# Optimization experiments

Measured on AMD Instinct MI355X. Metric: run time of the kernel, lower is better.

## Reference

```python
import jax, jax.numpy as jnp
import numpy as np

B, T, D, V, E = 128, 256, 1024, 32000, 300


def setup_inputs() -> dict:
    key = jax.random.key(0)
    ks = jax.random.split(key, 9)
    s = lambda d: 1.0 / np.sqrt(d)
    return {
        "input_to_decoder": jax.random.randint(ks[0], (B, 1), 0, V),
        "encoder_output": jax.random.normal(ks[1], (B, T, D), jnp.float32) * s(D),
        "state_h": jax.random.normal(ks[2], (B, D), jnp.float32) * s(D),
        "state_c": jax.random.normal(ks[3], (B, D), jnp.float32) * s(D),
        "emb_table": jax.random.normal(ks[4], (V, E), jnp.float32) * 0.02,
        "W_lstm": jax.random.normal(ks[5], (D + E, 4 * D), jnp.float32) * s(D + E),
        "U_lstm": jax.random.normal(ks[6], (D, 4 * D), jnp.float32) * s(D),
        "b_lstm": jnp.zeros((4 * D,), jnp.float32),
        "W_dense": jax.random.normal(ks[7], (D, V), jnp.float32) * s(D),
        "b_dense": jnp.zeros((V,), jnp.float32),
    }


def reference(input_to_decoder, encoder_output, state_h, state_c,
              emb_table, W_lstm, U_lstm, b_lstm, W_dense, b_dense):
    # embedding lookup + squeeze(axis=1): [B,1] -> [B,E]
    emb = emb_table[input_to_decoder[:, 0]]
    # Bahdanau-style dot scores: [B,T]
    scores = jnp.einsum("btd,bd->bt", encoder_output, state_h)
    # NOTE: faithful to source - context uses RAW (pre-softmax) scores
    context = jnp.einsum("btd,bt->bd", encoder_output, scores)  # [B,D]
    attention_weights = jax.nn.softmax(scores, axis=1)[..., None]  # [B,T,1]
    # concat context + embedding, single LSTM cell step (Keras gate order i,f,g,o)
    x = jnp.concatenate([context, emb], axis=1)  # [B,D+E]
    z = x @ W_lstm + state_h @ U_lstm + b_lstm  # [B,4D]
    zi, zf, zg, zo = jnp.split(z, 4, axis=1)
    c_new = jax.nn.sigmoid(zf) * state_c + jax.nn.sigmoid(zi) * jnp.tanh(zg)
    h_new = jax.nn.sigmoid(zo) * jnp.tanh(c_new)
    logits = h_new @ W_dense + b_dense  # [B,V]
    return logits, h_new, c_new, attention_weights, context
```

## Files before the change

### kernel.cpp

```cpp
#include <hip/hip_runtime.h>
#include <hip/hip_bf16.h>
#include <cmath>


#define Bc 128
#define Tc 256
#define Dc 1024
#define Vc 32000
#define Ec 300
#define KREAL 2348
#define KXP 2816
#define KSPLIT 4
#define N4 4096

typedef __attribute__((ext_vector_type(8))) short bf16x8;
typedef __attribute__((ext_vector_type(4))) float f32x4;

static __device__ __forceinline__ short f2bf(float x) {
    __hip_bfloat16 b = __float2bfloat16(x);
    return *reinterpret_cast<short*>(&b);
}
static __device__ __forceinline__ unsigned pack2(float a, float b) {
    return (unsigned)(unsigned short)f2bf(a) | ((unsigned)(unsigned short)f2bf(b) << 16);
}

__global__ void k_att1(const float* __restrict__ enc, const float* __restrict__ h,
                       float* __restrict__ scores_g, float* __restrict__ ctx_part) {
    const int tc = blockIdx.x;
    const int b  = blockIdx.y;
    const int tid = threadIdx.x;
    const int wave = tid >> 6, lane = tid & 63;
    __shared__ float s_acc[4][1024];

    const float4* h4 = (const float4*)(h + ((size_t)b << 10));
    float4 hv0 = h4[lane], hv1 = h4[lane + 64], hv2 = h4[lane + 128], hv3 = h4[lane + 192];

    float4 a0 = {0,0,0,0}, a1 = {0,0,0,0}, a2 = {0,0,0,0}, a3 = {0,0,0,0};
    const int t0 = (tc << 6) + (wave << 4);
    const float4* e4 = (const float4*)(enc + ((size_t)(b * Tc + t0) << 10));

    #pragma unroll 2
    for (int i = 0; i < 16; ++i) {
        float4 e0 = e4[lane], e1 = e4[lane + 64], e2 = e4[lane + 128], e3 = e4[lane + 192];
        e4 += 256;
        float d = e0.x*hv0.x + e0.y*hv0.y + e0.z*hv0.z + e0.w*hv0.w
                + e1.x*hv1.x + e1.y*hv1.y + e1.z*hv1.z + e1.w*hv1.w
                + e2.x*hv2.x + e2.y*hv2.y + e2.z*hv2.z + e2.w*hv2.w
                + e3.x*hv3.x + e3.y*hv3.y + e3.z*hv3.z + e3.w*hv3.w;
        #pragma unroll
        for (int off = 32; off; off >>= 1) d += __shfl_xor(d, off, 64);
        if (lane == 0) scores_g[(b << 8) + t0 + i] = d;
        a0.x += d*e0.x; a0.y += d*e0.y; a0.z += d*e0.z; a0.w += d*e0.w;
        a1.x += d*e1.x; a1.y += d*e1.y; a1.z += d*e1.z; a1.w += d*e1.w;
        a2.x += d*e2.x; a2.y += d*e2.y; a2.z += d*e2.z; a2.w += d*e2.w;
        a3.x += d*e3.x; a3.y += d*e3.y; a3.z += d*e3.z; a3.w += d*e3.w;
    }

    *(float4*)&s_acc[wave][lane << 2]         = a0;
    *(float4*)&s_acc[wave][256 + (lane << 2)] = a1;
    *(float4*)&s_acc[wave][512 + (lane << 2)] = a2;
    *(float4*)&s_acc[wave][768 + (lane << 2)] = a3;
    __syncthreads();
    float4 r0 = *(const float4*)&s_acc[0][tid << 2];
    float4 r1 = *(const float4*)&s_acc[1][tid << 2];
    float4 r2 = *(const float4*)&s_acc[2][tid << 2];
    float4 r3 = *(const float4*)&s_acc[3][tid << 2];
    float4 r;
    r.x = r0.x + r1.x + r2.x + r3.x;
    r.y = r0.y + r1.y + r2.y + r3.y;
    r.z = r0.z + r1.z + r2.z + r3.z;
    r.w = r0.w + r1.w + r2.w + r3.w;
    *(float4*)(ctx_part + (((size_t)(tc << 7) + b) << 10) + (tid << 2)) = r;
}

__global__ void k_att2(const float* __restrict__ ctx_part, const float* __restrict__ scores_g,
                       const int* __restrict__ idx, const float* __restrict__ emb_table,
                       const float* __restrict__ h,
                       float* __restrict__ ctx_out, float* __restrict__ attn_out,
                       unsigned short* __restrict__ x_bf) {
    const int b = blockIdx.x;
    const int tid = threadIdx.x;
    __shared__ float red[256];

    float4 cv = {0.f, 0.f, 0.f, 0.f};
    #pragma unroll
    for (int tc = 0; tc < 4; ++tc) {
        float4 s = *(const float4*)(ctx_part + (((size_t)(tc << 7) + b) << 10) + (tid << 2));
        cv.x += s.x; cv.y += s.y; cv.z += s.z; cv.w += s.w;
    }
    *(float4*)(ctx_out + ((size_t)b << 10) + (tid << 2)) = cv;

    unsigned short* xb = x_bf + (size_t)b * KXP;
    uint2 p0; p0.x = pack2(cv.x, cv.y); p0.y = pack2(cv.z, cv.w);
    *(uint2*)&xb[tid << 2] = p0;

    int row = idx[b];
    for (int i = tid; i < Ec; i += 256)
        xb[Dc + i] = (unsigned short)f2bf(emb_table[(size_t)row * Ec + i]);

    float4 hv = *(const float4*)(h + ((size_t)b << 10) + (tid << 2));
    uint2 p1; p1.x = pack2(hv.x, hv.y); p1.y = pack2(hv.z, hv.w);
    *(uint2*)&xb[(Dc + Ec) + (tid << 2)] = p1;

    for (int i = tid; i < KXP - KREAL; i += 256) xb[KREAL + i] = 0;

    float v = scores_g[(b << 8) + tid];
    red[tid] = v;
    __syncthreads();
    for (int s = 128; s; s >>= 1) { if (tid < s) red[tid] = fmaxf(red[tid], red[tid + s]); __syncthreads(); }
    float m = red[0];
    __syncthreads();
    float e = __expf(v - m);
    red[tid] = e;
    __syncthreads();
    for (int s = 128; s; s >>= 1) { if (tid < s) red[tid] += red[tid + s]; __syncthreads(); }
    attn_out[(b << 8) + tid] = e / red[0];
}

__global__ __launch_bounds__(512) void k_zgemm_mfma(
        const unsigned short* __restrict__ xbf, const float* __restrict__ Wl,
        const float* __restrict__ Ul, float* __restrict__ z_part) {
    __shared__ __align__(16) short blds[2 * 8 * 64 * 8];
    const int tid  = threadIdx.x;
    const int wid  = tid >> 6;
    const int lane = tid & 63;
    const int g    = lane >> 4;
    const int r    = lane & 15;
    const int n0   = blockIdx.x << 6;
    const int ksp  = blockIdx.y;

    const int pr = tid >> 4;
    const int c  = tid & 15;
    const int kk = (pr << 1) & 31;
    const int gg = kk >> 3, jj = kk & 7;
    const int ks0 = pr >> 4;

    f32x4 acc[4] = {};
    const unsigned short* xrow = xbf + (size_t)((wid << 4) + r) * KXP;

    float4 wra[2], wrb[2];
    bf16x8 areg[2][2];

    auto loadWU = [&](int gk) -> float4 {
        if (gk < 1324) return *(const float4*)(Wl + (size_t)gk * N4 + n0 + (c << 2));
        if (gk < KREAL) return *(const float4*)(Ul + (size_t)(gk - 1324) * N4 + n0 + (c << 2));
        return float4{0.f, 0.f, 0.f, 0.f};
    };

    {
        const int kt = (ksp * 11) << 6;
        wra[0] = loadWU(kt + (pr << 1));
        wrb[0] = loadWU(kt + (pr << 1) + 1);
        areg[0][0] = *(const bf16x8*)&xrow[kt + (g << 3)];
        areg[0][1] = *(const bf16x8*)&xrow[kt + 32 + (g << 3)];
    }

    #pragma unroll
    for (int t = 0; t < 11; ++t) {
        const int cur = t & 1;
        const int coff = cur << 12;
        {
            const float av[4] = {wra[cur].x, wra[cur].y, wra[cur].z, wra[cur].w};
            const float bv[4] = {wrb[cur].x, wrb[cur].y, wrb[cur].z, wrb[cur].w};
            #pragma unroll
            for (int i = 0; i < 4; ++i) {
                int n = (c << 2) + i;
                int nt = n >> 4;
                int inner = (gg << 4) | (n & 15);
                int Xs = ((((ks0 << 2) + nt) << 6) | inner) ^ nt;
                *(unsigned*)&blds[coff + (Xs << 3) + jj] = pack2(av[i], bv[i]);
            }
        }
        if (t < 10) {
            const int kt = ((ksp * 11) + t + 1) << 6;
            wra[cur ^ 1] = loadWU(kt + (pr << 1));
            wrb[cur ^ 1] = loadWU(kt + (pr << 1) + 1);
            areg[cur ^ 1][0] = *(const bf16x8*)&xrow[kt + (g << 3)];
            areg[cur ^ 1][1] = *(const bf16x8*)&xrow[kt + 32 + (g << 3)];
        }
        __syncthreads();
        #pragma unroll
        for (int ks = 0; ks < 2; ++ks) {
            #pragma unroll
            for (int nt = 0; nt < 4; ++nt) {
                int Xs = ((((ks << 2) + nt) << 6) | lane) ^ nt;
                bf16x8 bfr = *(const bf16x8*)&blds[coff + (Xs << 3)];
                acc[nt] = __builtin_amdgcn_mfma_f32_16x16x32_bf16(areg[cur][ks], bfr, acc[nt], 0, 0, 0);
            }
        }
        __syncthreads();
    }

    float* zp = z_part + ((size_t)ksp << 19);
    #pragma unroll
    for (int nt = 0; nt < 4; ++nt) {
        int col = n0 + (nt << 4) + r;
        #pragma unroll
        for (int j = 0; j < 4; ++j) {
            int rowm = (wid << 4) + (g << 2) + j;
            zp[((size_t)rowm << 12) + col] = acc[nt][j];
        }
    }
}

__global__ void k_gates(const float* __restrict__ z_part, const float* __restrict__ b_lstm,
                        const float* __restrict__ c_in, float* __restrict__ h_new,
                        float* __restrict__ c_new, unsigned short* __restrict__ h_bf) {
    int i = blockIdx.x * 256 + threadIdx.x;
    int b = i >> 8, d4 = (i & 255) << 2;
    size_t base = ((size_t)b << 12) + d4;
    float4 zi = *(const float4*)(b_lstm + d4);
    float4 zf = *(const float4*)(b_lstm + d4 + 1024);
    float4 zg = *(const float4*)(b_lstm + d4 + 2048);
    float4 zo = *(const float4*)(b_lstm + d4 + 3072);
    #pragma unroll
    for (int ks = 0; ks < KSPLIT; ++ks) {
        const float* zp = z_part + ((size_t)ks << 19);
        float4 t;
        t = *(const float4*)(zp + base);        zi.x += t.x; zi.y += t.y; zi.z += t.z; zi.w += t.w;
        t = *(const float4*)(zp + base + 1024); zf.x += t.x; zf.y += t.y; zf.z += t.z; zf.w += t.w;
        t = *(const float4*)(zp + base + 2048); zg.x += t.x; zg.y += t.y; zg.z += t.z; zg.w += t.w;
        t = *(const float4*)(zp + base + 3072); zo.x += t.x; zo.y += t.y; zo.z += t.z; zo.w += t.w;
    }
    float4 cin = *(const float4*)(c_in + ((size_t)b << 10) + d4);
    float4 cn, hn;
    {
        float si = 1.f/(1.f+__expf(-zi.x)), sf = 1.f/(1.f+__expf(-zf.x)), so = 1.f/(1.f+__expf(-zo.x));
        cn.x = sf*cin.x + si*tanhf(zg.x); hn.x = so*tanhf(cn.x);
        si = 1.f/(1.f+__expf(-zi.y)); sf = 1.f/(1.f+__expf(-zf.y)); so = 1.f/(1.f+__expf(-zo.y));
        cn.y = sf*cin.y + si*tanhf(zg.y); hn.y = so*tanhf(cn.y);
        si = 1.f/(1.f+__expf(-zi.z)); sf = 1.f/(1.f+__expf(-zf.z)); so = 1.f/(1.f+__expf(-zo.z));
        cn.z = sf*cin.z + si*tanhf(zg.z); hn.z = so*tanhf(cn.z);
        si = 1.f/(1.f+__expf(-zi.w)); sf = 1.f/(1.f+__expf(-zf.w)); so = 1.f/(1.f+__expf(-zo.w));
        cn.w = sf*cin.w + si*tanhf(zg.w); hn.w = so*tanhf(cn.w);
    }
    *(float4*)(c_new + ((size_t)b << 10) + d4) = cn;
    *(float4*)(h_new + ((size_t)b << 10) + d4) = hn;
    uint2 hp; hp.x = pack2(hn.x, hn.y); hp.y = pack2(hn.z, hn.w);
    *(uint2*)&h_bf[((size_t)b << 10) + d4] = hp;
}

__global__ __launch_bounds__(512, 4) void k_logits_mfma(
        const unsigned short* __restrict__ hbf, const float* __restrict__ Wd,
        const float* __restrict__ bd, float* __restrict__ out) {
    __shared__ __align__(16) short blds[2 * 16 * 64 * 8];
    const int tid  = threadIdx.x;
    const int wid  = tid >> 6;
    const int lane = tid & 63;
    const int g    = lane >> 4;
    const int r    = lane & 15;
    const int n0   = blockIdx.x << 6;

    const int pr = tid >> 4;
    const int c  = tid & 15;
    const int kk = (pr << 1) & 31;
    const int gg = kk >> 3, jj = kk & 7;
    const int ksA = pr >> 4;
    const int ksB = ksA + 2;

    f32x4 acc[4] = {};
    const unsigned short* hrow = hbf + ((size_t)((wid << 4) + r) << 10);
    const float* wbase = Wd + (size_t)(pr << 1) * Vc + n0 + (c << 2);

    float4 wra[2], wrb[2], wrc[2], wrd[2];
    bf16x8 areg[2][4];

    {
        wra[0] = *(const float4*)(wbase);
        wrb[0] = *(const float4*)(wbase + Vc);
        wrc[0] = *(const float4*)(wbase + (size_t)64 * Vc);
        wrd[0] = *(const float4*)(wbase + (size_t)65 * Vc);
        #pragma unroll
        for (int ks = 0; ks < 4; ++ks)
            areg[0][ks] = *(const bf16x8*)&hrow[(ks << 5) + (g << 3)];
    }

    #pragma unroll
    for (int t = 0; t < 8; ++t) {
        const int cur = t & 1;
        const int coff = cur << 13;
        {
            const float a0[4] = {wra[cur].x, wra[cur].y, wra[cur].z, wra[cur].w};
            const float b0[4] = {wrb[cur].x, wrb[cur].y, wrb[cur].z, wrb[cur].w};
            const float c0[4] = {wrc[cur].x, wrc[cur].y, wrc[cur].z, wrc[cur].w};
            const float d0[4] = {wrd[cur].x, wrd[cur].y, wrd[cur].z, wrd[cur].w};
            #pragma unroll
            for (int i = 0; i < 4; ++i) {
                int n = (c << 2) + i;
                int nt = n >> 4;
                int inner = (gg << 4) | (n & 15);
                int XsA = ((((ksA << 2) + nt) << 6) | inner) ^ nt;
                int XsB = ((((ksB << 2) + nt) << 6) | inner) ^ nt;
                *(unsigned*)&blds[coff + (XsA << 3) + jj] = pack2(a0[i], b0[i]);
                *(unsigned*)&blds[coff + (XsB << 3) + jj] = pack2(c0[i], d0[i]);
            }
        }
        if (t < 7) {
            const float* wb2 = wbase + (size_t)((t + 1) << 7) * Vc;
            wra[cur ^ 1] = *(const float4*)(wb2);
            wrb[cur ^ 1] = *(const float4*)(wb2 + Vc);
            wrc[cur ^ 1] = *(const float4*)(wb2 + (size_t)64 * Vc);
            wrd[cur ^ 1] = *(const float4*)(wb2 + (size_t)65 * Vc);
            #pragma unroll
            for (int ks = 0; ks < 4; ++ks)
                areg[cur ^ 1][ks] = *(const bf16x8*)&hrow[((t + 1) << 7) + (ks << 5) + (g << 3)];
        }
        __syncthreads();
        #pragma unroll
        for (int ks = 0; ks < 4; ++ks) {
            #pragma unroll
            for (int nt = 0; nt < 4; ++nt) {
                int Xs = ((((ks << 2) + nt) << 6) | lane) ^ nt;
                bf16x8 bfr = *(const bf16x8*)&blds[coff + (Xs << 3)];
                acc[nt] = __builtin_amdgcn_mfma_f32_16x16x32_bf16(areg[cur][ks], bfr, acc[nt], 0, 0, 0);
            }
        }
        __syncthreads();
    }

    #pragma unroll
    for (int nt = 0; nt < 4; ++nt) {
        int col = n0 + (nt << 4) + r;
        float bias = bd[col];
        #pragma unroll
        for (int j = 0; j < 4; ++j) {
            int row = (wid << 4) + (g << 2) + j;
            out[(size_t)row * Vc + col] = acc[nt][j] + bias;
        }
    }
}

extern "C" void kernel_launch(void* const* d_in, const int* in_sizes, int n_in,
                              void* d_out, int out_size, void* d_ws, size_t ws_size,
                              hipStream_t stream) {
    const int*   idx = (const int*)d_in[0];
    const float* enc = (const float*)d_in[1];
    const float* h   = (const float*)d_in[2];
    const float* c   = (const float*)d_in[3];
    const float* emb = (const float*)d_in[4];
    const float* Wl  = (const float*)d_in[5];
    const float* Ul  = (const float*)d_in[6];
    const float* bl  = (const float*)d_in[7];
    const float* Wd  = (const float*)d_in[8];
    const float* bd  = (const float*)d_in[9];

    float* out    = (float*)d_out;
    float* logits = out;
    float* h_new  = out + 4096000;
    float* c_new  = out + 4227072;
    float* attn   = out + 4358144;
    float* ctx    = out + 4390912;

    float*          ctx_part = out;
    float*          scores_g = out + 524288;
    float*          z_part   = out;
    unsigned short* x_bf16   = (unsigned short*)d_ws;
    unsigned short* h_bf16   = (unsigned short*)d_ws + 360448;

    hipLaunchKernelGGL(k_att1, dim3(4, 128), dim3(256), 0, stream, enc, h, scores_g, ctx_part);
    hipLaunchKernelGGL(k_att2, dim3(128), dim3(256), 0, stream, ctx_part, scores_g, idx, emb, h,
                       ctx, attn, x_bf16);
    hipLaunchKernelGGL(k_zgemm_mfma, dim3(64, KSPLIT), dim3(512), 0, stream, x_bf16, Wl, Ul, z_part);
    hipLaunchKernelGGL(k_gates, dim3(128), dim3(256), 0, stream, z_part, bl, c, h_new, c_new, h_bf16);
    hipLaunchKernelGGL(k_logits_mfma, dim3(500), dim3(512), 0, stream, h_bf16, Wd, bd, logits);
}
```

Measured before the change: 97.35 us.

## Deepen weight register prefetch to three stages and drop trailing barrier in GEMMs

Both the LSTM gate GEMM and the logits GEMM now prefetch fp32 weight tiles three iterations ahead into a rotating register ring. Activation fragments stay double-buffered. The trailing __syncthreads per k-step is removed; the double-buffered LDS plus the single leading barrier is relied on to keep writes and reads from racing. The logits kernel also halves its k-tile from 128 to 64 (16 steps), halves its LDS footprint and drops the min-blocks launch bound. The goal is more outstanding global loads and fewer barriers to hide memory latency on these bandwidth-bound weight streams, at the cost of more registers and more loop iterations.

```diff
diff --git a/kernel.cpp b/kernel.cpp
--- a/kernel.cpp
+++ b/kernel.cpp
@@ -128,6 +128,7 @@
     const int r    = lane & 15;
     const int n0   = blockIdx.x << 6;
     const int ksp  = blockIdx.y;
+    const int kbase = ksp * 11;
 
     const int pr = tid >> 4;
     const int c  = tid & 15;
@@ -138,7 +139,7 @@
     f32x4 acc[4] = {};
     const unsigned short* xrow = xbf + (size_t)((wid << 4) + r) * KXP;
 
-    float4 wra[2], wrb[2];
+    float4 wrA[3], wrB[3];
     bf16x8 areg[2][2];
 
     auto loadWU = [&](int gk) -> float4 {
@@ -147,21 +148,26 @@
         return float4{0.f, 0.f, 0.f, 0.f};
     };
 
+    #pragma unroll
+    for (int p = 0; p < 3; ++p) {
+        const int kt = (kbase + p) << 6;
+        wrA[p] = loadWU(kt + (pr << 1));
+        wrB[p] = loadWU(kt + (pr << 1) + 1);
+    }
     {
-        const int kt = (ksp * 11) << 6;
-        wra[0] = loadWU(kt + (pr << 1));
-        wrb[0] = loadWU(kt + (pr << 1) + 1);
+        const int kt = kbase << 6;
         areg[0][0] = *(const bf16x8*)&xrow[kt + (g << 3)];
         areg[0][1] = *(const bf16x8*)&xrow[kt + 32 + (g << 3)];
     }
 
     #pragma unroll
     for (int t = 0; t < 11; ++t) {
-        const int cur = t & 1;
+        const int slot = t % 3;
+        const int cur  = t & 1;
         const int coff = cur << 12;
         {
-            const float av[4] = {wra[cur].x, wra[cur].y, wra[cur].z, wra[cur].w};
-            const float bv[4] = {wrb[cur].x, wrb[cur].y, wrb[cur].z, wrb[cur].w};
+            const float av[4] = {wrA[slot].x, wrA[slot].y, wrA[slot].z, wrA[slot].w};
+            const float bv[4] = {wrB[slot].x, wrB[slot].y, wrB[slot].z, wrB[slot].w};
             #pragma unroll
             for (int i = 0; i < 4; ++i) {
                 int n = (c << 2) + i;
@@ -171,10 +177,13 @@
                 *(unsigned*)&blds[coff + (Xs << 3) + jj] = pack2(av[i], bv[i]);
             }
         }
-        if (t < 10) {
-            const int kt = ((ksp * 11) + t + 1) << 6;
-            wra[cur ^ 1] = loadWU(kt + (pr << 1));
-            wrb[cur ^ 1] = loadWU(kt + (pr << 1) + 1);
+        if (t + 3 < 11) {
+            const int kt = (kbase + t + 3) << 6;
+            wrA[slot] = loadWU(kt + (pr << 1));
+            wrB[slot] = loadWU(kt + (pr << 1) + 1);
+        }
+        if (t + 1 < 11) {
+            const int kt = (kbase + t + 1) << 6;
             areg[cur ^ 1][0] = *(const bf16x8*)&xrow[kt + (g << 3)];
             areg[cur ^ 1][1] = *(const bf16x8*)&xrow[kt + 32 + (g << 3)];
         }
@@ -188,7 +197,6 @@
                 acc[nt] = __builtin_amdgcn_mfma_f32_16x16x32_bf16(areg[cur][ks], bfr, acc[nt], 0, 0, 0);
             }
         }
-        __syncthreads();
     }
 
     float* zp = z_part + ((size_t)ksp << 19);
@@ -240,10 +248,10 @@
     *(uint2*)&h_bf[((size_t)b << 10) + d4] = hp;
 }
 
-__global__ __launch_bounds__(512, 4) void k_logits_mfma(
+__global__ __launch_bounds__(512) void k_logits_mfma(
         const unsigned short* __restrict__ hbf, const float* __restrict__ Wd,
         const float* __restrict__ bd, float* __restrict__ out) {
-    __shared__ __align__(16) short blds[2 * 16 * 64 * 8];
+    __shared__ __align__(16) short blds[2 * 8 * 64 * 8];
     const int tid  = threadIdx.x;
     const int wid  = tid >> 6;
     const int lane = tid & 63;
@@ -255,59 +263,54 @@
     const int c  = tid & 15;
     const int kk = (pr << 1) & 31;
     const int gg = kk >> 3, jj = kk & 7;
-    const int ksA = pr >> 4;
-    const int ksB = ksA + 2;
+    const int ks0 = pr >> 4;
 
     f32x4 acc[4] = {};
     const unsigned short* hrow = hbf + ((size_t)((wid << 4) + r) << 10);
     const float* wbase = Wd + (size_t)(pr << 1) * Vc + n0 + (c << 2);
 
-    float4 wra[2], wrb[2], wrc[2], wrd[2];
-    bf16x8 areg[2][4];
-
-    {
-        wra[0] = *(const float4*)(wbase);
-        wrb[0] = *(const float4*)(wbase + Vc);
-        wrc[0] = *(const float4*)(wbase + (size_t)64 * Vc);
-        wrd[0] = *(const float4*)(wbase + (size_t)65 * Vc);
-        #pragma unroll
-        for (int ks = 0; ks < 4; ++ks)
-            areg[0][ks] = *(const bf16x8*)&hrow[(ks << 5) + (g << 3)];
-    }
-
-    #pragma unroll
-    for (int t = 0; t < 8; ++t) {
-        const int cur = t & 1;
-        const int coff = cur << 13;
+    float4 wrA[3], wrB[3];
+    bf16x8 areg[2][2];
+
+    #pragma unroll
+    for (int p = 0; p < 3; ++p) {
+        const float* w0 = wbase + (size_t)(p << 6) * Vc;
+        wrA[p] = *(const float4*)(w0);
+        wrB[p] = *(const float4*)(w0 + Vc);
+    }
+    areg[0][0] = *(const bf16x8*)&hrow[(g << 3)];
+    areg[0][1] = *(const bf16x8*)&hrow[32 + (g << 3)];
+
+    #pragma unroll
+    for (int t = 0; t < 16; ++t) {
+        const int slot = t % 3;
+        const int cur  = t & 1;
+        const int coff = cur << 12;
         {
-            const float a0[4] = {wra[cur].x, wra[cur].y, wra[cur].z, wra[cur].w};
-            const float b0[4] = {wrb[cur].x, wrb[cur].y, wrb[cur].z, wrb[cur].w};
-            const float c0[4] = {wrc[cur].x, wrc[cur].y, wrc[cur].z, wrc[cur].w};
-            const float d0[4] = {wrd[cur].x, wrd[cur].y, wrd[cur].z, wrd[cur].w};
+            const float av[4] = {wrA[slot].x, wrA[slot].y, wrA[slot].z, wrA[slot].w};
+            const float bv[4] = {wrB[slot].x, wrB[slot].y, wrB[slot].z, wrB[slot].w};
             #pragma unroll
             for (int i = 0; i < 4; ++i) {
                 int n = (c << 2) + i;
                 int nt = n >> 4;
                 int inner = (gg << 4) | (n & 15);
-                int XsA = ((((ksA << 2) + nt) << 6) | inner) ^ nt;
-                int XsB = ((((ksB << 2) + nt) << 6) | inner) ^ nt;
-                *(unsigned*)&blds[coff + (XsA << 3) + jj] = pack2(a0[i], b0[i]);
-                *(unsigned*)&blds[coff + (XsB << 3) + jj] = pack2(c0[i], d0[i]);
+                int Xs = ((((ks0 << 2) + nt) << 6) | inner) ^ nt;
+                *(unsigned*)&blds[coff + (Xs << 3) + jj] = pack2(av[i], bv[i]);
             }
         }
-        if (t < 7) {
-            const float* wb2 = wbase + (size_t)((t + 1) << 7) * Vc;
-            wra[cur ^ 1] = *(const float4*)(wb2);
-            wrb[cur ^ 1] = *(const float4*)(wb2 + Vc);
-            wrc[cur ^ 1] = *(const float4*)(wb2 + (size_t)64 * Vc);
-            wrd[cur ^ 1] = *(const float4*)(wb2 + (size_t)65 * Vc);
-            #pragma unroll
-            for (int ks = 0; ks < 4; ++ks)
-                areg[cur ^ 1][ks] = *(const bf16x8*)&hrow[((t + 1) << 7) + (ks << 5) + (g << 3)];
+        if (t + 3 < 16) {
+            const float* w0 = wbase + (size_t)((t + 3) << 6) * Vc;
+            wrA[slot] = *(const float4*)(w0);
+            wrB[slot] = *(const float4*)(w0 + Vc);
+        }
+        if (t + 1 < 16) {
+            const int kt = (t + 1) << 6;
+            areg[cur ^ 1][0] = *(const bf16x8*)&hrow[kt + (g << 3)];
+            areg[cur ^ 1][1] = *(const bf16x8*)&hrow[kt + 32 + (g << 3)];
         }
         __syncthreads();
         #pragma unroll
-        for (int ks = 0; ks < 4; ++ks) {
+        for (int ks = 0; ks < 2; ++ks) {
             #pragma unroll
             for (int nt = 0; nt < 4; ++nt) {
                 int Xs = ((((ks << 2) + nt) << 6) | lane) ^ nt;
@@ -315,7 +318,6 @@
                 acc[nt] = __builtin_amdgcn_mfma_f32_16x16x32_bf16(areg[cur][ks], bfr, acc[nt], 0, 0, 0);
             }
         }
-        __syncthreads();
     }
 
     #pragma unroll
```

Result: no change. 96.20 us (-1.2%).
